# Performance work log

Measured on AMD Instinct MI355X. Metric: run time of the kernel, lower is better.

The kernel has to match this reference:

```python
import jax, jax.numpy as jnp
import numpy as np

EMBED = 1024
HEADS = 16
HEAD_DIM = EMBED // HEADS


def _rope(t):
    # t: (B, S, H, D) -> rotary embedding applied over last dim (GPT-NeoX rotate-half)
    B, S, H, D = t.shape
    half = D // 2
    inv_freq = 1.0 / (10000.0 ** (jnp.arange(0, half, dtype=jnp.float32) / half))
    freqs = jnp.arange(S, dtype=jnp.float32)[:, None] * inv_freq[None, :]  # (S, half)
    cos = jnp.cos(freqs)[None, :, None, :]
    sin = jnp.sin(freqs)[None, :, None, :]
    t1, t2 = t[..., :half], t[..., half:]
    return jnp.concatenate([t1 * cos - t2 * sin, t2 * cos + t1 * sin], axis=-1)


def setup_inputs() -> dict:
    key = jax.random.key(0)
    k1, k2, k3 = jax.random.split(key, 3)
    B, S = 2, 2048
    x = jax.random.normal(k1, (B, S, EMBED), dtype=jnp.float32)
    attn_mask = jnp.ones((B, S), dtype=bool)
    w_qkv = jax.random.normal(k2, (EMBED, 3 * EMBED), dtype=jnp.float32) * (1.0 / np.sqrt(EMBED))
    w_out = jax.random.normal(k3, (EMBED, EMBED), dtype=jnp.float32) * (1.0 / np.sqrt(EMBED))
    return {"x": x, "attn_mask": attn_mask, "w_qkv": w_qkv, "w_out": w_out, "is_causal": 1}


def reference(x, attn_mask, w_qkv, w_out, is_causal):
    B, S, E = x.shape
    qkv = x @ w_qkv                                   # (B, S, 3E)
    q, k, v = jnp.split(qkv, 3, axis=-1)
    q = q.reshape(B, S, HEADS, HEAD_DIM)
    k = k.reshape(B, S, HEADS, HEAD_DIM)
    v = v.reshape(B, S, HEADS, HEAD_DIM)
    q = _rope(q)
    k = _rope(k)
    scale = 1.0 / np.sqrt(HEAD_DIM)
    scores = jnp.einsum('bqhd,bkhd->bhqk', q, k) * scale  # (B, H, S, S)
    neg = jnp.asarray(-1e30, dtype=scores.dtype)
    if is_causal:
        causal = jnp.tril(jnp.ones((S, S), dtype=bool))
        scores = jnp.where(causal[None, None], scores, neg)
    else:
        scores = jnp.where(attn_mask[:, None, None, :], scores, neg)
    attn = jax.nn.softmax(scores, axis=-1)
    y = jnp.einsum('bhqk,bkhd->bqhd', attn, v).reshape(B, S, E)
    return y @ w_out
```

## Files before the change

### kernel.cpp

```cpp
#include <hip/hip_runtime.h>
#include <hip/hip_bf16.h>
#include <stdint.h>

typedef float v4f __attribute__((ext_vector_type(4)));
typedef short v8s __attribute__((ext_vector_type(8)));
typedef short v4s __attribute__((ext_vector_type(4)));

#define LOG2E 1.44269504088896f
#define QSCALE (0.125f * LOG2E)
#define SOFTMAX_OFF 16.0f

__device__ __forceinline__ unsigned short f2bf(float f) {
    unsigned int u = __float_as_uint(f);
    u += 0x7fffu + ((u >> 16) & 1u);
    return (unsigned short)(u >> 16);
}

#define LDS_FENCE() __builtin_amdgcn_fence(__ATOMIC_ACQ_REL, "workgroup")

__device__ __forceinline__ void gload_lds16(const unsigned short* g, unsigned short* s) {
    __builtin_amdgcn_global_load_lds(
        (const __attribute__((address_space(1))) unsigned int*)g,
        (__attribute__((address_space(3))) unsigned int*)s, 16, 0, 0);
}

#define BAR()      asm volatile("s_barrier" ::: "memory")
#define VMWAIT(N)  asm volatile("s_waitcnt vmcnt(" #N ")" ::: "memory")

#define PIPE_BARRIER_KEEP4()                                   \
    do {                                                       \
        asm volatile("s_waitcnt vmcnt(4)" ::: "memory");       \
        __builtin_amdgcn_s_barrier();                          \
        asm volatile("" ::: "memory");                         \
    } while (0)
#define PIPE_BARRIER_DRAIN()                                   \
    do {                                                       \
        asm volatile("s_waitcnt vmcnt(0)" ::: "memory");       \
        __builtin_amdgcn_s_barrier();                          \
        asm volatile("" ::: "memory");                         \
    } while (0)

__global__ void k_prep(const float* __restrict__ x,
                       const float* __restrict__ w_qkv,
                       const float* __restrict__ w_out,
                       unsigned short* __restrict__ xb,
                       unsigned short* __restrict__ wqkvT,
                       unsigned short* __restrict__ woutT,
                       float2* __restrict__ rope) {
    __shared__ unsigned short tile[64][65];
    int id = blockIdx.x, t = threadIdx.x;
    if (id < 1024) {
        int base = id * 256 + t;
#pragma unroll
        for (int k = 0; k < 4; ++k) {
            int i = base + k * 262144;
            float4 v = ((const float4*)x)[i];
            ushort4 o;
            o.x = f2bf(v.x); o.y = f2bf(v.y); o.z = f2bf(v.z); o.w = f2bf(v.w);
            ((ushort4*)xb)[i] = o;
        }
        return;
    }
    id -= 1024;
    if (id < 256) {
        int idx = id * 256 + t;
        int s = idx >> 5, d = idx & 31;
        float inv = __expf(-(float)d * 0.28782313662425572f);
        float sn, cs;
        sincosf((float)s * inv, &sn, &cs);
        rope[idx] = make_float2(cs, sn);
        return;
    }
    id -= 256;
    const float* src; unsigned short* dst; int N, kb, nb;
    if (id < 768) { src = w_qkv; dst = wqkvT; N = 3072; nb = (id % 48) * 64; kb = (id / 48) * 64; }
    else { id -= 768; src = w_out; dst = woutT; N = 1024; nb = (id % 16) * 64; kb = (id / 16) * 64; }
    const int K = 1024;
    for (int i = 0; i < 16; ++i) {
        int e = t + i * 256;
        int n_l = e & 63, k_l = e >> 6;
        tile[n_l][k_l] = f2bf(src[(size_t)(kb + k_l) * N + nb + n_l]);
    }
    __syncthreads();
    for (int i = 0; i < 16; ++i) {
        int e = t + i * 256;
        int k_l = e & 63, n_l = e >> 6;
        dst[(size_t)(nb + n_l) * K + kb + k_l] = tile[n_l][k_l];
    }
}

__global__ __launch_bounds__(512, 2) void k_gemm_qkv(
    const unsigned short* __restrict__ A,
    const unsigned short* __restrict__ Bt,
    const float2* __restrict__ rope,
    unsigned short* __restrict__ Qg,
    unsigned short* __restrict__ Kg,
    unsigned short* __restrict__ Vt) {
    const int K = 1024;
    __shared__ __align__(16) union {
        struct { unsigned short Ab[2][256 * 64], Bb[2][256 * 64]; } g;
        unsigned short vt[4][64][264];
        unsigned short qk[8][128][66];
    } sm;
    const int t = threadIdx.x;
    const int w = t >> 6, l = t & 63, quad = l >> 4, ln = l & 15;
    const int wr = w >> 2, wc = w & 3;
    const int lid = blockIdx.y * 12 + blockIdx.x;
    const int swzb = (lid & 7) * 24 + (lid >> 3);
    const int mb = (swzb / 12) * 256, nb = (swzb % 12) * 256;
    const int lxr = l >> 3;
    const int swz = ((l & 7) ^ lxr) * 8;

    v4f acc[8][4];
#pragma unroll
    for (int i = 0; i < 8; ++i)
#pragma unroll
        for (int j = 0; j < 4; ++j) acc[i][j] = (v4f){0.f, 0.f, 0.f, 0.f};

    auto stageHT = [&](const unsigned short* src, int grow, int k0, unsigned short* lds) {
#pragma unroll
        for (int c = 0; c < 2; ++c) {
            int r0 = w * 16 + c * 8;
            gload_lds16(src + (size_t)(grow + r0 + lxr) * K + k0 + swz, lds + r0 * 64);
        }
    };
    auto frag = [&](const unsigned short* base, int row, int g16) -> v8s {
        return *(const v8s*)&base[row * 64 + ((g16 ^ (row & 7)) << 3)];
    };

    v8s aF[4][2], bF0[2][2], bF1[2][2];
    auto readA = [&](const unsigned short* Ap, int ih) {
#pragma unroll
        for (int ii = 0; ii < 4; ++ii) {
            int row = wr * 128 + (ih * 4 + ii) * 16 + ln;
#pragma unroll
            for (int kh = 0; kh < 2; ++kh) aF[ii][kh] = frag(Ap, row, kh * 4 + quad);
        }
    };
    auto readB = [&](const unsigned short* Bp, int jh, v8s (&bF)[2][2]) {
#pragma unroll
        for (int jj = 0; jj < 2; ++jj) {
            int row = wc * 64 + (jh * 2 + jj) * 16 + ln;
#pragma unroll
            for (int kh = 0; kh < 2; ++kh) bF[jj][kh] = frag(Bp, row, kh * 4 + quad);
        }
    };
    auto mfma16 = [&](v8s (&bF)[2][2], int ih, int jh) {
        __builtin_amdgcn_s_setprio(1);
#pragma unroll
        for (int ii = 0; ii < 4; ++ii)
#pragma unroll
            for (int jj = 0; jj < 2; ++jj) {
                v4f* ac = &acc[ih * 4 + ii][jh * 2 + jj];
                *ac = __builtin_amdgcn_mfma_f32_16x16x32_bf16(aF[ii][0], bF[jj][0], *ac, 0, 0, 0);
                *ac = __builtin_amdgcn_mfma_f32_16x16x32_bf16(aF[ii][1], bF[jj][1], *ac, 0, 0, 0);
            }
        __builtin_amdgcn_s_setprio(0);
    };

    const unsigned short* Ap0 = &sm.g.Ab[0][0];
    const unsigned short* Ap1 = &sm.g.Ab[1][0];
    const unsigned short* Bp0 = &sm.g.Bb[0][0];
    const unsigned short* Bp1 = &sm.g.Bb[1][0];

    stageHT(A,  mb,       0,  &sm.g.Ab[0][0]);
    stageHT(A,  mb + 128, 0,  &sm.g.Ab[0][128 * 64]);
    stageHT(Bt, nb,       0,  &sm.g.Bb[0][0]);
    stageHT(Bt, nb + 128, 0,  &sm.g.Bb[0][128 * 64]);
    stageHT(Bt, nb,       64, &sm.g.Bb[1][0]);
    stageHT(Bt, nb + 128, 64, &sm.g.Bb[1][128 * 64]);
    VMWAIT(4);
    BAR();

    for (int it = 0; it < 8; ++it) {
        const int c1k = (2 * it + 1) * 64, n0k = (2 * it + 2) * 64, n1k = (2 * it + 3) * 64;
        const bool pre = it < 7;
        readA(Ap0, 0); readB(Bp0, 0, bF0);
        stageHT(A, mb, c1k, &sm.g.Ab[1][0]);
        BAR();
        mfma16(bF0, 0, 0);
        BAR();
        readB(Bp0, 1, bF1);
        stageHT(A, mb + 128, c1k, &sm.g.Ab[1][128 * 64]);
        BAR();
        mfma16(bF1, 0, 1);
        BAR();
        readA(Ap0, 1);
        if (pre) stageHT(Bt, nb, n0k, &sm.g.Bb[0][0]);
        BAR();
        mfma16(bF0, 1, 0);
        BAR();
        if (pre) stageHT(Bt, nb + 128, n0k, &sm.g.Bb[0][128 * 64]);
        BAR();
        mfma16(bF1, 1, 1);
        if (pre) VMWAIT(4); else VMWAIT(0);
        BAR();
        readA(Ap1, 0); readB(Bp1, 0, bF0);
        if (pre) stageHT(A, mb, n0k, &sm.g.Ab[0][0]);
        BAR();
        mfma16(bF0, 0, 0);
        BAR();
        readB(Bp1, 1, bF1);
        if (pre) stageHT(A, mb + 128, n0k, &sm.g.Ab[0][128 * 64]);
        BAR();
        mfma16(bF1, 0, 1);
        BAR();
        readA(Ap1, 1);
        if (pre) stageHT(Bt, nb, n1k, &sm.g.Bb[1][0]);
        BAR();
        mfma16(bF0, 1, 0);
        BAR();
        if (pre) stageHT(Bt, nb + 128, n1k, &sm.g.Bb[1][128 * 64]);
        BAR();
        mfma16(bF1, 1, 1);
        if (pre) VMWAIT(4);
        BAR();
    }

    if (nb >= 2048) {
        __syncthreads();
#pragma unroll
        for (int i = 0; i < 8; ++i)
#pragma unroll
            for (int j = 0; j < 4; ++j) {
                int d = j * 16 + ln;
                int s0 = wr * 128 + i * 16 + quad * 4;
                ushort4 pk;
                pk.x = f2bf(acc[i][j][0]); pk.y = f2bf(acc[i][j][1]);
                pk.z = f2bf(acc[i][j][2]); pk.w = f2bf(acc[i][j][3]);
                *(ushort4*)&sm.vt[wc][d][s0] = pk;
            }
        __syncthreads();
        const int hbase = (nb & 1023) >> 6;
        const int b = mb >> 11, sbase = mb & 2047;
#pragma unroll
        for (int i = 0; i < 16; ++i) {
            int c = t + i * 512;
            int h2 = c >> 11, dd = (c >> 5) & 63, off = (c & 31) * 8;
            v8s val = *(const v8s*)&sm.vt[h2][dd][off];
            *(v8s*)(Vt + ((size_t)((b * 16 + hbase + h2) * 64 + dd) * 2048 + sbase + off)) = val;
        }
        return;
    }

    const int nbw = nb + wc * 64;
    const int region = nbw >> 10;
    const int h = (nbw & 1023) >> 6;
    unsigned short* dst = region == 0 ? Qg : Kg;
    const float scale = region == 0 ? QSCALE : 1.0f;
    unsigned short* qkw = &sm.qk[w][0][0];
#pragma unroll
    for (int jj = 0; jj < 2; ++jj) {
        const float2* rp = rope + jj * 16 + ln;
#pragma unroll
        for (int i = 0; i < 8; ++i)
#pragma unroll
            for (int r = 0; r < 4; ++r) {
                int lr = i * 16 + quad * 4 + r;
                int s = (mb + wr * 128 + lr) & 2047;
                float2 cs = rp[s * 32];
                float t1 = acc[i][jj][r], t2 = acc[i][jj + 2][r];
                qkw[lr * 66 + jj * 16 + ln]      = f2bf((t1 * cs.x - t2 * cs.y) * scale);
                qkw[lr * 66 + jj * 16 + ln + 32] = f2bf((t2 * cs.x + t1 * cs.y) * scale);
            }
    }
    LDS_FENCE();
    const int row0 = mb + wr * 128;
    const int bb = row0 >> 11, s0 = row0 & 2047;
    unsigned short* gbase = dst + ((size_t)(bb * 16 + h) * 2048 + s0) * 64;
#pragma unroll
    for (int itn = 0; itn < 16; ++itn) {
        int c = itn * 64 + l;
        int lr = c >> 3, off = (c & 7) * 8;
        v8s val = *(const v8s*)&qkw[lr * 66 + off];
        *(v8s*)(gbase + (size_t)lr * 64 + off) = val;
    }
}

__global__ __launch_bounds__(256) void k_gemm_out(
    const unsigned short* __restrict__ A,
    const unsigned short* __restrict__ Bt,
    float* __restrict__ C) {
    const int K = 1024, N = 1024;
    __shared__ __align__(16) unsigned short Ab[3][4096];
    __shared__ __align__(16) unsigned short Bb[3][4096];
    const int t = threadIdx.x;
    const int w = t >> 6, l = t & 63, quad = l >> 4, ln = l & 15;
    const int wm = (w >> 1) * 64, wn = (w & 1) * 64;
    const int mb = blockIdx.y * 128, nb = blockIdx.x * 128;

    v4f acc[4][4];
#pragma unroll
    for (int i = 0; i < 4; ++i)
#pragma unroll
        for (int j = 0; j < 4; ++j) acc[i][j] = (v4f){0.f, 0.f, 0.f, 0.f};

    auto stage = [&](int buf, int k0) {
#pragma unroll
        for (int u = 0; u < 2; ++u) {
            int e = t + u * 256;
            gload_lds16(A + (size_t)(mb + (e >> 2)) * K + k0 + (e & 3) * 8,
                        &Ab[buf][(w * 64 + u * 256) * 8]);
            gload_lds16(Bt + (size_t)(nb + (e >> 2)) * K + k0 + (e & 3) * 8,
                        &Bb[buf][(w * 64 + u * 256) * 8]);
        }
    };

    stage(0, 0);
    stage(1, 32);
    int cur = 0, nxt = 2;
    for (int itk = 0; itk < 32; ++itk) {
        if (itk < 31) PIPE_BARRIER_KEEP4();
        else          PIPE_BARRIER_DRAIN();
        if (itk + 2 < 32) {
            stage(nxt, (itk + 2) * 32);
            nxt = nxt == 2 ? 0 : nxt + 1;
        }
        v8s af[4], bfr[4];
#pragma unroll
        for (int i = 0; i < 4; ++i)
            af[i] = *(const v8s*)&Ab[cur][(wm + i * 16 + ln) * 32 + quad * 8];
#pragma unroll
        for (int j = 0; j < 4; ++j)
            bfr[j] = *(const v8s*)&Bb[cur][(wn + j * 16 + ln) * 32 + quad * 8];
#pragma unroll
        for (int i = 0; i < 4; ++i)
#pragma unroll
            for (int j = 0; j < 4; ++j)
                acc[i][j] = __builtin_amdgcn_mfma_f32_16x16x32_bf16(
                    af[i], bfr[j], acc[i][j], 0, 0, 0);
        cur = cur == 2 ? 0 : cur + 1;
    }

#pragma unroll
    for (int i = 0; i < 4; ++i) {
        int r0 = mb + wm + i * 16 + quad * 4;
#pragma unroll
        for (int j = 0; j < 4; ++j) {
            int c0 = nb + wn + j * 16 + ln;
#pragma unroll
            for (int r = 0; r < 4; ++r)
                C[(size_t)(r0 + r) * N + c0] = acc[i][j][r];
        }
    }
}

__global__ __launch_bounds__(256, 4) void k_flash(
    const unsigned short* __restrict__ Qg,
    const unsigned short* __restrict__ Kg,
    const unsigned short* __restrict__ Vt,
    unsigned short* __restrict__ Og) {
    __shared__ __align__(16) unsigned short Kb[2][64 * 64];
    __shared__ __align__(16) unsigned short Vb[2][64 * 64];

    const int id = blockIdx.x;
    const int xcd = id & 7, slot = id >> 3;
    const int bh = xcd * 4 + (slot & 3);
    const int qt = 31 - (slot >> 2);
    const int qbase = qt * 64;
    const int nit = qt + 1;

    const int t = threadIdx.x, w = t >> 6, l = t & 63, quad = l >> 4, ln = l & 15;
    const int b = bh >> 4, h = bh & 15;

    const unsigned short* Qp = Qg + (size_t)bh * 2048 * 64;
    const unsigned short* Kp = Kg + (size_t)bh * 2048 * 64;
    const unsigned short* Vp = Vt + (size_t)bh * 64 * 2048;

    unsigned kst[2], vst[2];
    int cchunk = l & 7, rloc = l >> 3;
#pragma unroll
    for (int j = 0; j < 2; ++j) {
        int c = w + j * 4;
        int rr = c * 8 + rloc;
        int g = (cchunk + rr) & 7;
        kst[j] = (unsigned)(rr * 64 + g * 8);
        vst[j] = (unsigned)(rr * 2048 + g * 8);
    }
    const int c0 = ((quad - ln) & 7) * 8;
    const int c1 = ((quad + 4 - ln) & 7) * 8;
    int vch[4];
#pragma unroll
    for (int kt = 0; kt < 4; ++kt)
        vch[kt] = ((kt * 2 + (quad >> 1) - ln) & 7) * 8;
    const v4s ones4 = {0x3F80, 0x3F80, 0x3F80, 0x3F80};

    const int qrow = qbase + w * 16 + ln;
    v8s qf0 = *(const v8s*)(Qp + (size_t)qrow * 64 + quad * 8);
    v8s qf1 = *(const v8s*)(Qp + (size_t)qrow * 64 + quad * 8 + 32);

    v4f oacc[5];
#pragma unroll
    for (int dt = 0; dt < 5; ++dt) oacc[dt] = (v4f){0.f, 0.f, 0.f, 0.f};

    auto stage = [&](int buf, int kvb) {
        const unsigned short* kg = Kp + (size_t)kvb * 64;
        const unsigned short* vg = Vp + kvb;
#pragma unroll
        for (int j = 0; j < 2; ++j) {
            int c = w + j * 4;
            gload_lds16(kg + kst[j], &Kb[buf][c * 512]);
            gload_lds16(vg + vst[j], &Vb[buf][c * 512]);
        }
    };

    auto compute = [&](int buf, int it) {
        v4f sc[4];
#pragma unroll
        for (int kt = 0; kt < 4; ++kt) {
            int row = kt * 16 + ln;
            v8s k0 = *(const v8s*)&Kb[buf][row * 64 + c0];
            v8s k1 = *(const v8s*)&Kb[buf][row * 64 + c1];
            sc[kt] = (v4f){0.f, 0.f, 0.f, 0.f};
            sc[kt] = __builtin_amdgcn_mfma_f32_16x16x32_bf16(k0, qf0, sc[kt], 0, 0, 0);
            sc[kt] = __builtin_amdgcn_mfma_f32_16x16x32_bf16(k1, qf1, sc[kt], 0, 0, 0);
        }
        if (it == qt) {
            int qg = w * 16 + ln;
#pragma unroll
            for (int kt = 0; kt < 4; ++kt) {
                int kv = kt * 16 + quad * 4;
#pragma unroll
                for (int r = 0; r < 4; ++r)
                    if (kv + r > qg) sc[kt][r] = -1e30f;
            }
        }
#pragma unroll
        for (int kt = 0; kt < 4; ++kt)
#pragma unroll
            for (int r = 0; r < 4; ++r)
                sc[kt][r] = exp2f(sc[kt][r] - SOFTMAX_OFF);

        v4s pa[4];
#pragma unroll
        for (int kt = 0; kt < 4; ++kt) {
            union { __hip_bfloat162 hh; unsigned int u; } p01, p23;
            p01.hh = __float22bfloat162_rn(make_float2(sc[kt][0], sc[kt][1]));
            p23.hh = __float22bfloat162_rn(make_float2(sc[kt][2], sc[kt][3]));
            union { v4s v; unsigned int u[2]; } pk;
            pk.u[0] = p01.u; pk.u[1] = p23.u;
            pa[kt] = pk.v;
        }
        __builtin_amdgcn_s_setprio(1);
#pragma unroll
        for (int dt = 0; dt < 4; ++dt) {
            int rowb = (dt * 16 + ln) * 64;
#pragma unroll
            for (int kt = 0; kt < 4; ++kt) {
                v8s vv = *(const v8s*)&Vb[buf][rowb + vch[kt]];
                v4s lo = __builtin_shufflevector(vv, vv, 0, 1, 2, 3);
                v4s hi = __builtin_shufflevector(vv, vv, 4, 5, 6, 7);
                v4s vf = (quad & 1) ? hi : lo;
                oacc[dt] = __builtin_amdgcn_mfma_f32_16x16x16bf16_1k(pa[kt], vf, oacc[dt], 0, 0, 0);
            }
        }
#pragma unroll
        for (int kt = 0; kt < 4; ++kt)
            oacc[4] = __builtin_amdgcn_mfma_f32_16x16x16bf16_1k(pa[kt], ones4, oacc[4], 0, 0, 0);
        __builtin_amdgcn_s_setprio(0);
    };

    stage(0, 0);
    for (int it = 0;;) {
        const int buf = it & 1;
        stage(buf ^ 1, (it + 1) * 64);
        VMWAIT(4);
        BAR();
        compute(buf, it);
        if (++it >= nit) break;
        BAR();
    }

    float rden[4];
#pragma unroll
    for (int r = 0; r < 4; ++r) rden[r] = 1.f / oacc[4][r];
#pragma unroll
    for (int dt = 0; dt < 4; ++dt)
#pragma unroll
        for (int r = 0; r < 4; ++r) {
            int s = qbase + w * 16 + quad * 4 + r;
            Og[(size_t)(b * 2048 + s) * 1024 + h * 64 + dt * 16 + ln] =
                f2bf(oacc[dt][r] * rden[r]);
        }
}

extern "C" void kernel_launch(void* const* d_in, const int* in_sizes, int n_in,
                              void* d_out, int out_size, void* d_ws, size_t ws_size,
                              hipStream_t stream) {
    const float* x     = (const float*)d_in[0];
    const float* w_qkv = (const float*)d_in[2];
    const float* w_out = (const float*)d_in[3];
    char* ws = (char*)d_ws;

    unsigned short* xb    = (unsigned short*)(ws);
    unsigned short* wqkvT = (unsigned short*)(ws + (size_t)(8 << 20));
    unsigned short* woutT = (unsigned short*)(ws + (size_t)(14 << 20));
    unsigned short* Qg    = (unsigned short*)(ws + (size_t)(16 << 20));
    unsigned short* Kg    = (unsigned short*)(ws + (size_t)(24 << 20));
    unsigned short* Vt    = (unsigned short*)(ws + (size_t)(32 << 20));
    unsigned short* Og    = (unsigned short*)(ws + (size_t)(40 << 20));
    float2*         rope  = (float2*)(ws + (size_t)(48 << 20));

    k_prep<<<2304, 256, 0, stream>>>(x, w_qkv, w_out, xb, wqkvT, woutT, rope);
    k_gemm_qkv<<<dim3(12, 16), 512, 0, stream>>>(xb, wqkvT, rope, Qg, Kg, Vt);
    k_flash<<<1024, 256, 0, stream>>>(Qg, Kg, Vt, Og);
    k_gemm_out<<<dim3(8, 32), 256, 0, stream>>>(Og, woutT, (float*)d_out);
}
```

Measured before the change: 189.7 us.

## Retile output GEMM with swizzled LDS, vectorize weight transpose, trim flash ops

The output projection GEMM now uses 64x128 tiles with a K-step of 64 and an XOR-swizzled LDS layout. This doubles the block count and should cut LDS bank conflicts. The weight transpose in the prep kernel reads float4 and writes 16-byte vectors instead of scalar elements. The flash kernel folds the softmax offset into the MFMA accumulator init and loads only the needed 4-element V half instead of loading 8 and selecting. Together these remove several small costs across kernels, but the smaller GEMM tile gives less reuse per block.

```diff
diff --git a/kernel.cpp b/kernel.cpp
--- a/kernel.cpp
+++ b/kernel.cpp
@@ -26,19 +26,6 @@
 
 #define BAR()      asm volatile("s_barrier" ::: "memory")
 #define VMWAIT(N)  asm volatile("s_waitcnt vmcnt(" #N ")" ::: "memory")
-
-#define PIPE_BARRIER_KEEP4()                                   \
-    do {                                                       \
-        asm volatile("s_waitcnt vmcnt(4)" ::: "memory");       \
-        __builtin_amdgcn_s_barrier();                          \
-        asm volatile("" ::: "memory");                         \
-    } while (0)
-#define PIPE_BARRIER_DRAIN()                                   \
-    do {                                                       \
-        asm volatile("s_waitcnt vmcnt(0)" ::: "memory");       \
-        __builtin_amdgcn_s_barrier();                          \
-        asm volatile("" ::: "memory");                         \
-    } while (0)
 
 __global__ void k_prep(const float* __restrict__ x,
                        const float* __restrict__ w_qkv,
@@ -47,7 +34,7 @@
                        unsigned short* __restrict__ wqkvT,
                        unsigned short* __restrict__ woutT,
                        float2* __restrict__ rope) {
-    __shared__ unsigned short tile[64][65];
+    __shared__ __align__(16) unsigned short tile[64][88];
     int id = blockIdx.x, t = threadIdx.x;
     if (id < 1024) {
         int base = id * 256 + t;
@@ -76,16 +63,23 @@
     if (id < 768) { src = w_qkv; dst = wqkvT; N = 3072; nb = (id % 48) * 64; kb = (id / 48) * 64; }
     else { id -= 768; src = w_out; dst = woutT; N = 1024; nb = (id % 16) * 64; kb = (id / 16) * 64; }
     const int K = 1024;
-    for (int i = 0; i < 16; ++i) {
+#pragma unroll
+    for (int i = 0; i < 4; ++i) {
         int e = t + i * 256;
-        int n_l = e & 63, k_l = e >> 6;
-        tile[n_l][k_l] = f2bf(src[(size_t)(kb + k_l) * N + nb + n_l]);
+        int k_l = e >> 4, n4 = (e & 15) * 4;
+        float4 v = *(const float4*)&src[(size_t)(kb + k_l) * N + nb + n4];
+        tile[n4 + 0][k_l] = f2bf(v.x);
+        tile[n4 + 1][k_l] = f2bf(v.y);
+        tile[n4 + 2][k_l] = f2bf(v.z);
+        tile[n4 + 3][k_l] = f2bf(v.w);
     }
     __syncthreads();
-    for (int i = 0; i < 16; ++i) {
-        int e = t + i * 256;
-        int k_l = e & 63, n_l = e >> 6;
-        dst[(size_t)(nb + n_l) * K + kb + k_l] = tile[n_l][k_l];
+#pragma unroll
+    for (int i = 0; i < 2; ++i) {
+        int c = t + i * 256;
+        int n_l = c >> 3, kc = (c & 7) * 8;
+        v8s val = *(const v8s*)&tile[n_l][kc];
+        *(v8s*)&dst[(size_t)(nb + n_l) * K + kb + kc] = val;
     }
 }
 
@@ -282,58 +276,71 @@
     const unsigned short* __restrict__ Bt,
     float* __restrict__ C) {
     const int K = 1024, N = 1024;
-    __shared__ __align__(16) unsigned short Ab[3][4096];
-    __shared__ __align__(16) unsigned short Bb[3][4096];
+    __shared__ __align__(16) unsigned short Ab[3][64 * 64];
+    __shared__ __align__(16) unsigned short Bb[3][128 * 64];
     const int t = threadIdx.x;
     const int w = t >> 6, l = t & 63, quad = l >> 4, ln = l & 15;
-    const int wm = (w >> 1) * 64, wn = (w & 1) * 64;
-    const int mb = blockIdx.y * 128, nb = blockIdx.x * 128;
-
-    v4f acc[4][4];
-#pragma unroll
-    for (int i = 0; i < 4; ++i)
+    const int wm = (w >> 1) * 32, wn = (w & 1) * 64;
+    const int mb = blockIdx.y * 64, nb = blockIdx.x * 128;
+    const int lxr = l >> 3;
+    const int swz = ((l & 7) ^ lxr) * 8;
+
+    v4f acc[2][4];
+#pragma unroll
+    for (int i = 0; i < 2; ++i)
 #pragma unroll
         for (int j = 0; j < 4; ++j) acc[i][j] = (v4f){0.f, 0.f, 0.f, 0.f};
 
     auto stage = [&](int buf, int k0) {
 #pragma unroll
-        for (int u = 0; u < 2; ++u) {
-            int e = t + u * 256;
-            gload_lds16(A + (size_t)(mb + (e >> 2)) * K + k0 + (e & 3) * 8,
-                        &Ab[buf][(w * 64 + u * 256) * 8]);
-            gload_lds16(Bt + (size_t)(nb + (e >> 2)) * K + k0 + (e & 3) * 8,
-                        &Bb[buf][(w * 64 + u * 256) * 8]);
-        }
+        for (int c = 0; c < 2; ++c) {
+            int r0 = w * 16 + c * 8;
+            gload_lds16(A + (size_t)(mb + r0 + lxr) * K + k0 + swz, &Ab[buf][r0 * 64]);
+        }
+#pragma unroll
+        for (int c = 0; c < 4; ++c) {
+            int r0 = w * 32 + c * 8;
+            gload_lds16(Bt + (size_t)(nb + r0 + lxr) * K + k0 + swz, &Bb[buf][r0 * 64]);
+        }
+    };
+    auto frag = [&](const unsigned short* base, int row, int g16) -> v8s {
+        return *(const v8s*)&base[row * 64 + ((g16 ^ (row & 7)) << 3)];
     };
 
     stage(0, 0);
-    stage(1, 32);
+    stage(1, 64);
     int cur = 0, nxt = 2;
-    for (int itk = 0; itk < 32; ++itk) {
-        if (itk < 31) PIPE_BARRIER_KEEP4();
-        else          PIPE_BARRIER_DRAIN();
-        if (itk + 2 < 32) {
-            stage(nxt, (itk + 2) * 32);
+    for (int itk = 0; itk < 16; ++itk) {
+        if (itk < 15) VMWAIT(6);
+        else          VMWAIT(0);
+        BAR();
+        if (itk + 2 < 16) {
+            stage(nxt, (itk + 2) * 64);
             nxt = nxt == 2 ? 0 : nxt + 1;
         }
-        v8s af[4], bfr[4];
-#pragma unroll
-        for (int i = 0; i < 4; ++i)
-            af[i] = *(const v8s*)&Ab[cur][(wm + i * 16 + ln) * 32 + quad * 8];
+        v8s af[2][2], bf[4][2];
+#pragma unroll
+        for (int i = 0; i < 2; ++i)
+#pragma unroll
+            for (int kh = 0; kh < 2; ++kh)
+                af[i][kh] = frag(&Ab[cur][0], wm + i * 16 + ln, kh * 4 + quad);
 #pragma unroll
         for (int j = 0; j < 4; ++j)
-            bfr[j] = *(const v8s*)&Bb[cur][(wn + j * 16 + ln) * 32 + quad * 8];
-#pragma unroll
-        for (int i = 0; i < 4; ++i)
-#pragma unroll
-            for (int j = 0; j < 4; ++j)
-                acc[i][j] = __builtin_amdgcn_mfma_f32_16x16x32_bf16(
-                    af[i], bfr[j], acc[i][j], 0, 0, 0);
+#pragma unroll
+            for (int kh = 0; kh < 2; ++kh)
+                bf[j][kh] = frag(&Bb[cur][0], wn + j * 16 + ln, kh * 4 + quad);
+#pragma unroll
+        for (int i = 0; i < 2; ++i)
+#pragma unroll
+            for (int j = 0; j < 4; ++j) {
+                acc[i][j] = __builtin_amdgcn_mfma_f32_16x16x32_bf16(af[i][0], bf[j][0], acc[i][j], 0, 0, 0);
+                acc[i][j] = __builtin_amdgcn_mfma_f32_16x16x32_bf16(af[i][1], bf[j][1], acc[i][j], 0, 0, 0);
+            }
         cur = cur == 2 ? 0 : cur + 1;
     }
 
 #pragma unroll
-    for (int i = 0; i < 4; ++i) {
+    for (int i = 0; i < 2; ++i) {
         int r0 = mb + wm + i * 16 + quad * 4;
 #pragma unroll
         for (int j = 0; j < 4; ++j) {
@@ -379,10 +386,10 @@
     }
     const int c0 = ((quad - ln) & 7) * 8;
     const int c1 = ((quad + 4 - ln) & 7) * 8;
-    int vch[4];
+    int vcol[4];
 #pragma unroll
     for (int kt = 0; kt < 4; ++kt)
-        vch[kt] = ((kt * 2 + (quad >> 1) - ln) & 7) * 8;
+        vcol[kt] = (((kt * 2 + (quad >> 1) - ln) & 7) << 3) + (quad & 1) * 4;
     const v4s ones4 = {0x3F80, 0x3F80, 0x3F80, 0x3F80};
 
     const int qrow = qbase + w * 16 + ln;
@@ -411,7 +418,7 @@
             int row = kt * 16 + ln;
             v8s k0 = *(const v8s*)&Kb[buf][row * 64 + c0];
             v8s k1 = *(const v8s*)&Kb[buf][row * 64 + c1];
-            sc[kt] = (v4f){0.f, 0.f, 0.f, 0.f};
+            sc[kt] = (v4f){-SOFTMAX_OFF, -SOFTMAX_OFF, -SOFTMAX_OFF, -SOFTMAX_OFF};
             sc[kt] = __builtin_amdgcn_mfma_f32_16x16x32_bf16(k0, qf0, sc[kt], 0, 0, 0);
             sc[kt] = __builtin_amdgcn_mfma_f32_16x16x32_bf16(k1, qf1, sc[kt], 0, 0, 0);
         }
@@ -429,7 +436,7 @@
         for (int kt = 0; kt < 4; ++kt)
 #pragma unroll
             for (int r = 0; r < 4; ++r)
-                sc[kt][r] = exp2f(sc[kt][r] - SOFTMAX_OFF);
+                sc[kt][r] = exp2f(sc[kt][r]);
 
         v4s pa[4];
 #pragma unroll
@@ -447,10 +454,7 @@
             int rowb = (dt * 16 + ln) * 64;
 #pragma unroll
             for (int kt = 0; kt < 4; ++kt) {
-                v8s vv = *(const v8s*)&Vb[buf][rowb + vch[kt]];
-                v4s lo = __builtin_shufflevector(vv, vv, 0, 1, 2, 3);
-                v4s hi = __builtin_shufflevector(vv, vv, 4, 5, 6, 7);
-                v4s vf = (quad & 1) ? hi : lo;
+                v4s vf = *(const v4s*)&Vb[buf][rowb + vcol[kt]];
                 oacc[dt] = __builtin_amdgcn_mfma_f32_16x16x16bf16_1k(pa[kt], vf, oacc[dt], 0, 0, 0);
             }
         }
@@ -504,5 +508,5 @@
     k_prep<<<2304, 256, 0, stream>>>(x, w_qkv, w_out, xb, wqkvT, woutT, rope);
     k_gemm_qkv<<<dim3(12, 16), 512, 0, stream>>>(xb, wqkvT, rope, Qg, Kg, Vt);
     k_flash<<<1024, 256, 0, stream>>>(Qg, Kg, Vt, Og);
-    k_gemm_out<<<dim3(8, 32), 256, 0, stream>>>(Og, woutT, (float*)d_out);
-}
+    k_gemm_out<<<dim3(8, 64), 256, 0, stream>>>(Og, woutT, (float*)d_out);
+}
```

New measurement: 182.6 us. 1.04x faster.
